# Kernel tuning notes

Measured on AMD Instinct MI355X. Metric: run time of the kernel, lower is better.

Reference implementation:

```python
import jax, jax.numpy as jnp
import numpy as np

B, D, NH, HD = 32, 384, 8, 48
HP = WP = 14
N = HP * WP
L = 24
EPS_LN = 1e-5


def _ln(x, w, b):
    m = jnp.mean(x, -1, keepdims=True)
    v = jnp.mean((x - m) ** 2, -1, keepdims=True)
    return (x - m) * jax.lax.rsqrt(v + EPS_LN) * w + b


def _gelu(x):
    return jax.nn.gelu(x, approximate=False)


def _conv(x, w, s, p, groups=1):
    return jax.lax.conv_general_dilated(x, w, (s, s), [(p, p), (p, p)],
        dimension_numbers=('NCHW', 'OIHW', 'NCHW'), feature_group_count=groups)


def _bn(x, g, b):
    # eval-mode BatchNorm2d with running_mean=0, running_var=1
    scale = g * jax.lax.rsqrt(jnp.asarray(1.0 + 1e-5, x.dtype))
    return x * scale[None, :, None, None] + b[None, :, None, None]


def _pos_embed(pos_w, pos_b):
    two_pi = 2.0 * np.pi
    y = (jnp.arange(HP, dtype=jnp.float32) + 1.0) / ((HP + 1e-6) * two_pi)
    xg = (jnp.arange(WP, dtype=jnp.float32) + 1.0) / ((WP + 1e-6) * two_pi)
    y_embed = jnp.broadcast_to(y[:, None], (HP, WP))
    x_embed = jnp.broadcast_to(xg[None, :], (HP, WP))
    dim_t = 10000.0 ** (2.0 * (jnp.arange(32) // 2).astype(jnp.float32) / 32.0)
    px = x_embed[..., None] / dim_t  # [H,W,32]
    py = y_embed[..., None] / dim_t
    px = jnp.stack([jnp.sin(px[..., 0::2]), jnp.cos(px[..., 1::2])], -1).reshape(HP, WP, 32)
    py = jnp.stack([jnp.sin(py[..., 0::2]), jnp.cos(py[..., 1::2])], -1).reshape(HP, WP, 32)
    pos = jnp.concatenate([py, px], -1)  # [H,W,64]
    pos = jnp.einsum('hwc,dc->hwd', pos, pos_w[:, :, 0, 0]) + pos_b
    return pos.reshape(1, N, D)


def _xca_block(t, p):
    Bc = t.shape[0]
    h = _ln(t, p['n1_w'], p['n1_b'])
    qkv = (h @ p['qkv_w'].T + p['qkv_b']).reshape(Bc, N, 3, NH, HD)
    q = qkv[:, :, 0].transpose(0, 2, 3, 1)  # [B,H,d,N]
    k = qkv[:, :, 1].transpose(0, 2, 3, 1)
    v = qkv[:, :, 2].transpose(0, 2, 3, 1)
    q = q / jnp.maximum(jnp.linalg.norm(q, axis=-1, keepdims=True), 1e-12)
    k = k / jnp.maximum(jnp.linalg.norm(k, axis=-1, keepdims=True), 1e-12)
    attn = jnp.einsum('bhdn,bhen->bhde', q, k) * p['temp'][None, :, None, None]
    a = jax.nn.softmax(attn, -1)  # channel-wise softmax over d_h
    o = jnp.einsum('bhde,bhen->bnhd', a, v).reshape(Bc, N, D)
    o = o @ p['proj_w'].T + p['proj_b']
    t = t + p['g1'] * o
    h = _ln(t, p['n3_w'], p['n3_b']).transpose(0, 2, 1).reshape(Bc, D, HP, WP)
    h = _conv(h, p['lpi1_w'], 1, 1, groups=D) + p['lpi1_b'][None, :, None, None]
    h = _bn(_gelu(h), p['lpi_bn_g'], p['lpi_bn_b'])
    h = _conv(h, p['lpi2_w'], 1, 1, groups=D) + p['lpi2_b'][None, :, None, None]
    t = t + p['g3'] * h.reshape(Bc, D, N).transpose(0, 2, 1)
    h = _ln(t, p['n2_w'], p['n2_b'])
    h = _gelu(h @ p['fc1_w'].T + p['fc1_b']) @ p['fc2_w'].T + p['fc2_b']
    return t + p['g2'] * h


def _ca_block(t, p):
    Bc, Nc, _ = t.shape
    h = _ln(t, p['n1_w'], p['n1_b'])
    qkv = (h @ p['qkv_w'].T + p['qkv_b']).reshape(Bc, Nc, 3, NH, HD)
    q = qkv[:, :, 0].transpose(0, 2, 1, 3)  # [B,H,N,d]
    k = qkv[:, :, 1].transpose(0, 2, 1, 3)
    v = qkv[:, :, 2].transpose(0, 2, 1, 3)
    attn = jnp.sum(q[:, :, :1] * k, -1) * (HD ** -0.5)  # [B,H,N]
    a = jax.nn.softmax(attn, -1)
    cls = jnp.einsum('bhn,bhnd->bhd', a, v).reshape(Bc, 1, D)
    cls = cls @ p['proj_w'].T + p['proj_b']
    attn_out = jnp.concatenate([cls, h[:, 1:]], 1)
    t = t + p['g1'] * attn_out
    t = _ln(t, p['n2_w'], p['n2_b'])
    res = t
    cls2 = _gelu(t[:, :1] @ p['fc1_w'].T + p['fc1_b']) @ p['fc2_w'].T + p['fc2_b']
    return jnp.concatenate([p['g2'] * cls2, t[:, 1:]], 1) + res


def setup_inputs() -> dict:
    key = jax.random.key(0)
    k = iter(jax.random.split(key, 64))
    def rn(shape, std=0.02):
        return jax.random.normal(next(k), shape, jnp.float32) * std
    inp = {}
    inp['x'] = jax.random.normal(next(k), (B, 3, 224, 224), jnp.float32)
    inp['cls_token'] = rn((1, 1, D))
    inp['pos_w'] = rn((D, 64, 1, 1))
    inp['pos_b'] = jnp.zeros((D,))
    for i, (co, ci) in enumerate([(48, 3), (96, 48), (192, 96), (384, 192)], 1):
        inp['pe_w%d' % i] = rn((co, ci, 3, 3))
        inp['pe_g%d' % i] = jnp.ones((co,))
        inp['pe_b%d' % i] = jnp.zeros((co,))
    inp['xqkv_w'] = rn((L, 3 * D, D)); inp['xqkv_b'] = jnp.zeros((L, 3 * D))
    inp['xproj_w'] = rn((L, D, D)); inp['xproj_b'] = jnp.zeros((L, D))
    inp['xtemp'] = jnp.ones((L, NH))
    for n in ('n1', 'n2', 'n3'):
        inp['x%s_w' % n] = jnp.ones((L, D)); inp['x%s_b' % n] = jnp.zeros((L, D))
    inp['xfc1_w'] = rn((L, 4 * D, D)); inp['xfc1_b'] = jnp.zeros((L, 4 * D))
    inp['xfc2_w'] = rn((L, D, 4 * D)); inp['xfc2_b'] = jnp.zeros((L, D))
    inp['xlpi1_w'] = rn((L, D, 1, 3, 3), 0.1); inp['xlpi1_b'] = jnp.zeros((L, D))
    inp['xlpi2_w'] = rn((L, D, 1, 3, 3), 0.1); inp['xlpi2_b'] = jnp.zeros((L, D))
    inp['xbn_g'] = jnp.ones((L, D)); inp['xbn_b'] = jnp.zeros((L, D))
    for g in ('g1', 'g2', 'g3'):
        inp['x%s' % g] = jnp.full((L, D), 1e-5)
    L2 = 2
    inp['cqkv_w'] = rn((L2, 3 * D, D)); inp['cqkv_b'] = jnp.zeros((L2, 3 * D))
    inp['cproj_w'] = rn((L2, D, D)); inp['cproj_b'] = jnp.zeros((L2, D))
    for n in ('n1', 'n2'):
        inp['c%s_w' % n] = jnp.ones((L2, D)); inp['c%s_b' % n] = jnp.zeros((L2, D))
    inp['cfc1_w'] = rn((L2, 4 * D, D)); inp['cfc1_b'] = jnp.zeros((L2, 4 * D))
    inp['cfc2_w'] = rn((L2, D, 4 * D)); inp['cfc2_b'] = jnp.zeros((L2, D))
    inp['cg1'] = jnp.full((L2, D), 1e-5); inp['cg2'] = jnp.full((L2, D), 1e-5)
    inp['norm_w'] = jnp.ones((D,)); inp['norm_b'] = jnp.zeros((D,))
    inp['head_w'] = rn((1000, D)); inp['head_b'] = jnp.zeros((1000,))
    return inp


def reference(x, cls_token, pos_w, pos_b, pe_w1, pe_g1, pe_b1, pe_w2, pe_g2, pe_b2, pe_w3, pe_g3, pe_b3, pe_w4, pe_g4, pe_b4, xqkv_w, xqkv_b, xproj_w, xproj_b, xtemp, xn1_w, xn1_b, xn2_w, xn2_b, xn3_w, xn3_b, xfc1_w, xfc1_b, xfc2_w, xfc2_b, xlpi1_w, xlpi1_b, xlpi2_w, xlpi2_b, xbn_g, xbn_b, xg1, xg2, xg3, cqkv_w, cqkv_b, cproj_w, cproj_b, cn1_w, cn1_b, cn2_w, cn2_b, cfc1_w, cfc1_b, cfc2_w, cfc2_b, cg1, cg2, norm_w, norm_b, head_w, head_b):
    h = _gelu(_bn(_conv(x, pe_w1, 2, 1), pe_g1, pe_b1))
    h = _gelu(_bn(_conv(h, pe_w2, 2, 1), pe_g2, pe_b2))
    h = _gelu(_bn(_conv(h, pe_w3, 2, 1), pe_g3, pe_b3))
    h = _bn(_conv(h, pe_w4, 2, 1), pe_g4, pe_b4)  # [B,D,14,14]
    t = h.reshape(h.shape[0], D, N).transpose(0, 2, 1)  # [B,N,D]
    t = t + _pos_embed(pos_w, pos_b)
    xca = {'qkv_w': xqkv_w, 'qkv_b': xqkv_b, 'proj_w': xproj_w, 'proj_b': xproj_b,
           'temp': xtemp, 'n1_w': xn1_w, 'n1_b': xn1_b, 'n2_w': xn2_w, 'n2_b': xn2_b,
           'n3_w': xn3_w, 'n3_b': xn3_b, 'fc1_w': xfc1_w, 'fc1_b': xfc1_b,
           'fc2_w': xfc2_w, 'fc2_b': xfc2_b, 'lpi1_w': xlpi1_w, 'lpi1_b': xlpi1_b,
           'lpi2_w': xlpi2_w, 'lpi2_b': xlpi2_b, 'lpi_bn_g': xbn_g, 'lpi_bn_b': xbn_b,
           'g1': xg1, 'g2': xg2, 'g3': xg3}
    t, _ = jax.lax.scan(lambda c, p: (_xca_block(c, p), None), t, xca)
    t = jnp.concatenate([jnp.broadcast_to(cls_token, (t.shape[0], 1, D)), t], 1)
    for i in range(2):
        p = {'qkv_w': cqkv_w[i], 'qkv_b': cqkv_b[i], 'proj_w': cproj_w[i],
             'proj_b': cproj_b[i], 'n1_w': cn1_w[i], 'n1_b': cn1_b[i],
             'n2_w': cn2_w[i], 'n2_b': cn2_b[i], 'fc1_w': cfc1_w[i],
             'fc1_b': cfc1_b[i], 'fc2_w': cfc2_w[i], 'fc2_b': cfc2_b[i],
             'g1': cg1[i], 'g2': cg2[i]}
        t = _ca_block(t, p)
    t = _ln(t, norm_w, norm_b)[:, 0]
    return t @ head_w.T + head_b
```

## Files before the change

### kernel.cpp

```cpp
#include <hip/hip_runtime.h>
#include <hip/hip_bf16.h>

#define B_ 32
#define D_ 384
#define N_ 196
#define NH_ 8
#define HD_ 48
#define L_ 24

typedef __bf16 bf16x8 __attribute__((ext_vector_type(8)));
typedef __bf16 bf16x4 __attribute__((ext_vector_type(4)));
typedef float f32x4 __attribute__((ext_vector_type(4)));

__device__ __forceinline__ float gelu_f(float v){
    return 0.5f * v * (1.0f + erff(v * 0.70710678118654752f));
}

__global__ __launch_bounds__(256) void cvt_bf(const float* __restrict__ s, __bf16* __restrict__ d, long n){
    long i = ((long)blockIdx.x * 256 + threadIdx.x) * 8;
    if (i >= n) return;
    float4 a = *reinterpret_cast<const float4*>(s + i);
    float4 b = *reinterpret_cast<const float4*>(s + i + 4);
    bf16x8 r;
    r[0] = (__bf16)a.x; r[1] = (__bf16)a.y; r[2] = (__bf16)a.z; r[3] = (__bf16)a.w;
// ... 84 lines not shown
            int p = i * 256 + tid;
            int r = p >> 2, cq = p & 3;
            *reinterpret_cast<bf16x8*>(Ab + r * 80 + cq * 16) = i ? vaC1 : vaC0;
            *reinterpret_cast<bf16x8*>(Bb + r * 80 + cq * 16) = i ? vwC1 : vwC0;
        }
        __syncthreads();
        int kn = (k0 + 32 < Kpad) ? k0 + 32 : k0;
        bf16x8 vaN0 = loadA(kn, 0), vaN1 = loadA(kn, 1);
        bf16x8 vwN0 = loadB(kn, 0), vwN1 = loadB(kn, 1);
        bf16x8 af[4], bfr[4];
        #pragma unroll
        for (int m = 0; m < 4; m++)
            af[m] = *reinterpret_cast<const bf16x8*>(Ab + (wm * 64 + m * 16 + lo) * 80 + hi * 16);
        #pragma unroll
        for (int n = 0; n < 4; n++)
            bfr[n] = *reinterpret_cast<const bf16x8*>(Bb + (wn * 64 + n * 16 + lo) * 80 + hi * 16);
        #pragma unroll
        for (int m = 0; m < 4; m++)
            #pragma unroll
            for (int n = 0; n < 4; n++)
                acc[m][n] = __builtin_amdgcn_mfma_f32_16x16x32_bf16(af[m], bfr[n], acc[m][n], 0, 0, 0);
        __syncthreads();
        vaC0 = vaN0; vaC1 = vaN1; vwC0 = vwN0; vwC1 = vwN1;
    }
    float* Cf = (float*)Cv;
    __bf16* Cb = (__bf16*)Cv;
    #pragma unroll
    for (int m = 0; m < 4; m++){
        #pragma unroll
        for (int n = 0; n < 4; n++){
            int row = row0 + wm * 64 + m * 16 + hi * 4;
            int col = col0 + wn * 64 + n * 16 + lo;
            if (col >= N) continue;
            float scale = g[col] * rsqrtf(1.0f + 1e-5f);
            float bv = bb[col];
            #pragma unroll
            for (int j = 0; j < 4; j++){
                float v = acc[m][n][j] * scale + bv;
                if (GELU) v = gelu_f(v);
                if (POSOUT)
                    Cf[(long)(row + j) * 384 + col] = v + pos[((row + j) % 196) * 384 + col];
                else
                    Cb[(long)(row + j) * N + col] = (__bf16)v;
            }
        }
    }
}

template<int GELU, int POSOUT, int C, int Hi, int Wi, int Ho, int Wo>
__global__ __launch_bounds__(256) void gemm_cig(const __bf16* __restrict__ in, int Kpad,
                                                const __bf16* __restrict__ W,
                                                const float* __restrict__ g, const float* __restrict__ bb,
                                                void* __restrict__ Cv, int N,
                                                const float* __restrict__ pos){
    __shared__ __align__(16) char smem[36864];
    char* Ab = smem;
    char* Bb = smem + 18432;
    const int tid  = threadIdx.x;
    const int lane = tid & 63;
    const int wn   = (tid >> 6) & 1;
    const int wm   = tid >> 7;
    const int row0 = blockIdx.x * 128;
    const int col0 = blockIdx.y * 128;
    const int hi = lane >> 4, lo = lane & 15;
    f32x4 acc[4][4] = {};
    auto loadA = [&](int kk, int i)->bf16x8 {
        int p = i * 256 + tid;
        int r = p >> 3, cq = p & 7;
        int koff = kk + cq * 8;
        int tap = koff / C;
        int ci = koff - tap * C;
        bf16x8 va{};
        if (tap < 9){
            int pix = row0 + r;
            int b = pix / (Ho * Wo);
            int rem = pix - b * (Ho * Wo);
            int oy = rem / Wo, ox = rem - oy * Wo;
            int iy = oy * 2 - 1 + tap / 3, ix = ox * 2 - 1 + tap % 3;
            if ((unsigned)iy < (unsigned)Hi && (unsigned)ix < (unsigned)Wi)
                va = *reinterpret_cast<const bf16x8*>(in + (((long)b * Hi + iy) * Wi + ix) * C + ci);
        }
        return va;
    };
    auto loadB = [&](int kk, int i)->bf16x8 {
        int p = i * 256 + tid;
        int r = p >> 3, cq = p & 7;
        int gc = col0 + r;
        bf16x8 vw{};
        if (gc < N) vw = *reinterpret_cast<const bf16x8*>(W + (long)gc * Kpad + kk + cq * 8);
        return vw;
    };
    bf16x8 vaC[4], vwC[4];
    #pragma unroll
    for (int i = 0; i < 4; i++){ vaC[i] = loadA(0, i); vwC[i] = loadB(0, i); }
    for (int k0 = 0; k0 < Kpad; k0 += 64){
        #pragma unroll
        for (int i = 0; i < 4; i++){
            int p = i * 256 + tid;
            int r = p >> 3, cq = p & 7;
            *reinterpret_cast<bf16x8*>(Ab + r * 144 + cq * 16) = vaC[i];
            *reinterpret_cast<bf16x8*>(Bb + r * 144 + cq * 16) = vwC[i];
        }
        __syncthreads();
        int kn = (k0 + 64 < Kpad) ? k0 + 64 : k0;
        bf16x8 vaN[4], vwN[4];
        #pragma unroll
        for (int i = 0; i < 4; i++){ vaN[i] = loadA(kn, i); vwN[i] = loadB(kn, i); }
        bf16x8 af[2][4], bfr[2][4];
        #pragma unroll
        for (int m = 0; m < 4; m++){
            af[0][m] = *reinterpret_cast<const bf16x8*>(Ab + (wm * 64 + m * 16 + lo) * 144 + hi * 16);
            af[1][m] = *reinterpret_cast<const bf16x8*>(Ab + (wm * 64 + m * 16 + lo) * 144 + 64 + hi * 16);
        }
        #pragma unroll
        for (int n = 0; n < 4; n++){
            bfr[0][n] = *reinterpret_cast<const bf16x8*>(Bb + (wn * 64 + n * 16 + lo) * 144 + hi * 16);
            bfr[1][n] = *reinterpret_cast<const bf16x8*>(Bb + (wn * 64 + n * 16 + lo) * 144 + 64 + hi * 16);
        }
        #pragma unroll
        for (int kc = 0; kc < 2; kc++)
            #pragma unroll
            for (int m = 0; m < 4; m++)
                #pragma unroll
                for (int n = 0; n < 4; n++)
                    acc[m][n] = __builtin_amdgcn_mfma_f32_16x16x32_bf16(af[kc][m], bfr[kc][n], acc[m][n], 0, 0, 0);
        __syncthreads();
        #pragma unroll
        for (int i = 0; i < 4; i++){ vaC[i] = vaN[i]; vwC[i] = vwN[i]; }
    }
    float* Cf = (float*)Cv;
    __bf16* Cb = (__bf16*)Cv;
    #pragma unroll
    for (int m = 0; m < 4; m++){
        #pragma unroll
        for (int n = 0; n < 4; n++){
            int row = row0 + wm * 64 + m * 16 + hi * 4;
            int col = col0 + wn * 64 + n * 16 + lo;
            if (col >= N) continue;
            float scale = g[col] * rsqrtf(1.0f + 1e-5f);
            float bv = bb[col];
            #pragma unroll
            for (int j = 0; j < 4; j++){
                float v = acc[m][n][j] * scale + bv;
                if (GELU) v = gelu_f(v);
                if (POSOUT)
                    Cf[(long)(row + j) * 384 + col] = v + pos[((row + j) % 196) * 384 + col];
                else
                    Cb[(long)(row + j) * N + col] = (__bf16)v;
            }
        }
    }
}

__global__ __launch_bounds__(128) void ln384(const float* __restrict__ x, long xstride,
                                             const float* __restrict__ w, const float* __restrict__ b,
                                             float* __restrict__ y, long ystride){
    long row = blockIdx.x;
    int tid = threadIdx.x;
    const float* xr = x + row * xstride;
    float v0 = xr[tid], v1 = xr[tid + 128], v2 = xr[tid + 256];
    float s = v0 + v1 + v2;
    float ss = v0 * v0 + v1 * v1 + v2 * v2;
    for (int off = 32; off; off >>= 1){ s += __shfl_down(s, off); ss += __shfl_down(ss, off); }
    __shared__ float rs[2], rss[2];
    if ((tid & 63) == 0){ rs[tid >> 6] = s; rss[tid >> 6] = ss; }
    __syncthreads();
    float S = rs[0] + rs[1], SS = rss[0] + rss[1];
    float m = S * (1.0f / 384.0f);
    float var = SS * (1.0f / 384.0f) - m * m;
    float r = rsqrtf(var + 1e-5f);
    float* yr = y + row * ystride;
    yr[tid]       = (v0 - m) * r * w[tid]       + b[tid];
    yr[tid + 128] = (v1 - m) * r * w[tid + 128] + b[tid + 128];
    yr[tid + 256] = (v2 - m) * r * w[tid + 256] + b[tid + 256];
}

__global__ __launch_bounds__(128) void ln384_bf(const float* __restrict__ x,
                                                const float* __restrict__ w, const float* __restrict__ b,
                                                __bf16* __restrict__ y){
    long row = blockIdx.x;
    int tid = threadIdx.x;
    const float* xr = x + row * 384;
    float v0 = xr[tid], v1 = xr[tid + 128], v2 = xr[tid + 256];
    float s = v0 + v1 + v2;
    float ss = v0 * v0 + v1 * v1 + v2 * v2;
    for (int off = 32; off; off >>= 1){ s += __shfl_down(s, off); ss += __shfl_down(ss, off); }
    __shared__ float rs[2], rss[2];
    if ((tid & 63) == 0){ rs[tid >> 6] = s; rss[tid >> 6] = ss; }
    __syncthreads();
    float S = rs[0] + rs[1], SS = rss[0] + rss[1];
    float m = S * (1.0f / 384.0f);
    float var = SS * (1.0f / 384.0f) - m * m;
    float r = rsqrtf(var + 1e-5f);
    __bf16* yr = y + row * 384;
    yr[tid]       = (__bf16)((v0 - m) * r * w[tid]       + b[tid]);
    yr[tid + 128] = (__bf16)((v1 - m) * r * w[tid + 128] + b[tid + 128]);
    yr[tid + 256] = (__bf16)((v2 - m) * r * w[tid + 256] + b[tid + 256]);
}

__global__ __launch_bounds__(128) void proj_res_lnt(const __bf16* __restrict__ o2,
                                                    const float* __restrict__ g1,
                                                    float* __restrict__ t,
                                                    const float* __restrict__ n3w, const float* __restrict__ n3b,
                                                    __bf16* __restrict__ ht){
    long row = blockIdx.x;
    int tid = threadIdx.x;
    int c0 = tid * 4;
    float v[4] = {0.f, 0.f, 0.f, 0.f};
    if (tid < 96){
        float4 tv = *reinterpret_cast<const float4*>(t + row * 384 + c0);
        bf16x4 ov = *reinterpret_cast<const bf16x4*>(o2 + row * 384 + c0);
        v[0] = tv.x + g1[c0 + 0] * (float)ov[0];
        v[1] = tv.y + g1[c0 + 1] * (float)ov[1];
        v[2] = tv.z + g1[c0 + 2] * (float)ov[2];
        v[3] = tv.w + g1[c0 + 3] * (float)ov[3];
        *reinterpret_cast<float4*>(t + row * 384 + c0) = make_float4(v[0], v[1], v[2], v[3]);
    }
    float s = v[0] + v[1] + v[2] + v[3];
    float ss = v[0] * v[0] + v[1] * v[1] + v[2] * v[2] + v[3] * v[3];
    for (int off = 32; off; off >>= 1){ s += __shfl_down(s, off); ss += __shfl_down(ss, off); }
    __shared__ float rs[2], rss[2];
    if ((tid & 63) == 0){ rs[tid >> 6] = s; rss[tid >> 6] = ss; }
    __syncthreads();
    float S = rs[0] + rs[1], SS = rss[0] + rss[1];
    float m = S * (1.0f / 384.0f);
    float var = SS * (1.0f / 384.0f) - m * m;
    float r = rsqrtf(var + 1e-5f);
    if (tid < 96){
        int b = (int)(row / 196), n = (int)(row % 196);
        __bf16* yb = ht + ((long)b * 384) * 196 + n;
        #pragma unroll
        for (int j = 0; j < 4; j++){
            int c = c0 + j;
            yb[(long)c * 196] = (__bf16)((v[j] - m) * r * n3w[c] + n3b[c]);
        }
    }
}

__global__ __launch_bounds__(128) void ln2res(float* __restrict__ t,
                                              const __bf16* __restrict__ hadd,
                                              const float* __restrict__ n2w, const float* __restrict__ n2b,
                                              __bf16* __restrict__ h){
    long row = blockIdx.x;
    int tid = threadIdx.x;
    int c0 = tid * 4;
    float v[4] = {0.f, 0.f, 0.f, 0.f};
    if (tid < 96){
        float4 tv = *reinterpret_cast<const float4*>(t + row * 384 + c0);
        bf16x4 hv = *reinterpret_cast<const bf16x4*>(hadd + row * 384 + c0);
        v[0] = tv.x + (float)hv[0];
        v[1] = tv.y + (float)hv[1];
        v[2] = tv.z + (float)hv[2];
        v[3] = tv.w + (float)hv[3];
        *reinterpret_cast<float4*>(t + row * 384 + c0) = make_float4(v[0], v[1], v[2], v[3]);
    }
    float s = v[0] + v[1] + v[2] + v[3];
    float ss = v[0] * v[0] + v[1] * v[1] + v[2] * v[2] + v[3] * v[3];
    for (int off = 32; off; off >>= 1){ s += __shfl_down(s, off); ss += __shfl_down(ss, off); }
    __shared__ float rs[2], rss[2];
    if ((tid & 63) == 0){ rs[tid >> 6] = s; rss[tid >> 6] = ss; }
    __syncthreads();
    float S = rs[0] + rs[1], SS = rss[0] + rss[1];
    float m = S * (1.0f / 384.0f);
    float var = SS * (1.0f / 384.0f) - m * m;
    float r = rsqrtf(var + 1e-5f);
    if (tid < 96){
        bf16x4 o;
        #pragma unroll
        for (int j = 0; j < 4; j++){
            int c = c0 + j;
            o[j] = (__bf16)((v[j] - m) * r * n2w[c] + n2b[c]);
        }
        *reinterpret_cast<bf16x4*>(h + row * 384 + c0) = o;
    }
}

__global__ __launch_bounds__(128) void fc2_res_ln(const __bf16* __restrict__ f2,
                                                  const float* __restrict__ g2,
                                                  float* __restrict__ t,
                                                  const float* __restrict__ n1w, const float* __restrict__ n1b,
                                                  __bf16* __restrict__ h){
    long row = blockIdx.x;
    int tid = threadIdx.x;
    int c0 = tid * 4;
    float v[4] = {0.f, 0.f, 0.f, 0.f};
    if (tid < 96){
        float4 tv = *reinterpret_cast<const float4*>(t + row * 384 + c0);
        bf16x4 fv = *reinterpret_cast<const bf16x4*>(f2 + row * 384 + c0);
        v[0] = tv.x + g2[c0 + 0] * (float)fv[0];
        v[1] = tv.y + g2[c0 + 1] * (float)fv[1];
        v[2] = tv.z + g2[c0 + 2] * (float)fv[2];
        v[3] = tv.w + g2[c0 + 3] * (float)fv[3];
        *reinterpret_cast<float4*>(t + row * 384 + c0) = make_float4(v[0], v[1], v[2], v[3]);
    }
    float s = v[0] + v[1] + v[2] + v[3];
    float ss = v[0] * v[0] + v[1] * v[1] + v[2] * v[2] + v[3] * v[3];
    for (int off = 32; off; off >>= 1){ s += __shfl_down(s, off); ss += __shfl_down(ss, off); }
    __shared__ float rs[2], rss[2];
    if ((tid & 63) == 0){ rs[tid >> 6] = s; rss[tid >> 6] = ss; }
    __syncthreads();
    float S = rs[0] + rs[1], SS = rss[0] + rss[1];
    float m = S * (1.0f / 384.0f);
    float var = SS * (1.0f / 384.0f) - m * m;
    float r = rsqrtf(var + 1e-5f);
    if (tid < 96){
        bf16x4 o;
// ... 101 lines not shown
        for (int n = 0; n < 2; n++){
            int row = row0 + m * 16 + hi * 4;
            int col = col0 + wn * 32 + n * 16 + lo;
            if (NGUARD && col >= Ncols) continue;
            float bv = bias[col];
            #pragma unroll
            for (int j = 0; j < 4; j++){
                if (GUARD && (row + j) >= M) continue;
                float v = acc[m][n][j] + bv;
                if (MODE == 1) v = gelu_f(v);
                long ci = (long)(row + j) * ldc + col;
                if (OUTBF) Cb[ci] = (__bf16)v;
                else Cf[ci] = v;
            }
        }
    }
}

__global__ __launch_bounds__(256) void gemm_bb3(const __bf16* __restrict__ A, long lda,
                                                const __bf16* __restrict__ W, int Kw,
                                                const float* __restrict__ bias,
                                                __bf16* __restrict__ C, long ldc,
                                                int K){
    __shared__ __align__(16) char smem[18432];
    char* Ab = smem;
    char* Bb = smem + 9216;
    const int tid = threadIdx.x;
    const int lane = tid & 63;
    const int wid = tid >> 6;
    const int wm = wid >> 1, wnn = wid & 1;
    const int row0 = blockIdx.x * 64;
    const int col0 = blockIdx.y * 64;
    const int hi = lane >> 4, lo = lane & 15;
    f32x4 acc[2][2] = {};
    auto loadA = [&](int kk, int i)->bf16x8 {
        int p = i * 256 + tid;
        int r = p >> 3, cq = p & 7;
        return *reinterpret_cast<const bf16x8*>(A + (long)(row0 + r) * lda + kk + cq * 8);
    };
    auto loadB = [&](int kk, int i)->bf16x8 {
        int p = i * 256 + tid;
        int r = p >> 3, cq = p & 7;
        return *reinterpret_cast<const bf16x8*>(W + (long)(col0 + r) * Kw + kk + cq * 8);
    };
    bf16x8 vaC[2], vwC[2];
    vaC[0] = loadA(0, 0); vaC[1] = loadA(0, 1);
    vwC[0] = loadB(0, 0); vwC[1] = loadB(0, 1);
    for (int k0 = 0; k0 < K; k0 += 64){
        #pragma unroll
        for (int i = 0; i < 2; i++){
            int p = i * 256 + tid;
            int r = p >> 3, cq = p & 7;
            *reinterpret_cast<bf16x8*>(Ab + r * 144 + cq * 16) = vaC[i];
            *reinterpret_cast<bf16x8*>(Bb + r * 144 + cq * 16) = vwC[i];
        }
        __syncthreads();
        int kn = (k0 + 64 < K) ? k0 + 64 : k0;
        bf16x8 vaN[2], vwN[2];
        vaN[0] = loadA(kn, 0); vaN[1] = loadA(kn, 1);
        vwN[0] = loadB(kn, 0); vwN[1] = loadB(kn, 1);
        bf16x8 af[2][2], bfr[2][2];
        #pragma unroll
        for (int m = 0; m < 2; m++){
            af[0][m] = *reinterpret_cast<const bf16x8*>(Ab + (wm * 32 + m * 16 + lo) * 144 + hi * 16);
            af[1][m] = *reinterpret_cast<const bf16x8*>(Ab + (wm * 32 + m * 16 + lo) * 144 + 64 + hi * 16);
        }
        #pragma unroll
        for (int n = 0; n < 2; n++){
            bfr[0][n] = *reinterpret_cast<const bf16x8*>(Bb + (wnn * 32 + n * 16 + lo) * 144 + hi * 16);
            bfr[1][n] = *reinterpret_cast<const bf16x8*>(Bb + (wnn * 32 + n * 16 + lo) * 144 + 64 + hi * 16);
        }
        #pragma unroll
        for (int kc = 0; kc < 2; kc++)
            #pragma unroll
            for (int m = 0; m < 2; m++)
                #pragma unroll
                for (int n = 0; n < 2; n++)
                    acc[m][n] = __builtin_amdgcn_mfma_f32_16x16x32_bf16(af[kc][m], bfr[kc][n], acc[m][n], 0, 0, 0);
        __syncthreads();
        vaC[0] = vaN[0]; vaC[1] = vaN[1]; vwC[0] = vwN[0]; vwC[1] = vwN[1];
    }
    #pragma unroll
    for (int m = 0; m < 2; m++){
        #pragma unroll
        for (int n = 0; n < 2; n++){
            int row = row0 + wm * 32 + m * 16 + hi * 4;
            int col = col0 + wnn * 32 + n * 16 + lo;
            float bv = bias[col];
            #pragma unroll
            for (int j = 0; j < 4; j++)
                C[(long)(row + j) * ldc + col] = (__bf16)(acc[m][n][j] + bv);
        }
    }
}

__global__ __launch_bounds__(384) void pos_embed(const float* __restrict__ pw, const float* __restrict__ pb,
                                                 float* __restrict__ pos){
    __shared__ float p64[64];
    int n = blockIdx.x;
    int iy = n / 14, ix = n % 14;
    int t = threadIdx.x;
    if (t < 64){
        int axis = t >> 5;
        int c = t & 31;
        int u = c >> 1;
        float coord = (axis == 0) ? (float)(iy + 1) : (float)(ix + 1);
        float val = coord / ((14.0f + 1e-6f) * 6.283185307179586f);
        float T = powf(10000.0f, (float)u / 16.0f);
        float a = val / T;
        p64[t] = (c & 1) ? cosf(a) : sinf(a);
    }
    __syncthreads();
    float acc = 0.f;
    const float* wr = pw + (long)t * 64;
    #pragma unroll 8
    for (int c = 0; c < 64; c++) acc += p64[c] * wr[c];
    pos[n * 384 + t] = acc + pb[t];
}

__global__ __launch_bounds__(256) void xca2(const __bf16* __restrict__ qkv, const float* __restrict__ temp,
                                            __bf16* __restrict__ o){
    __shared__ __align__(16) char smem[45056];
    __bf16* qs = (__bf16*)smem;
    __bf16* ks = (__bf16*)(smem + 22272);
    float* inq = (float*)(smem + 44544);
    float* ink = (float*)(smem + 44736);
    float* att = (float*)smem;
    __bf16* abf = (__bf16*)(smem + 22272);
    int bh = blockIdx.x;
    int b = bh >> 3, h = bh & 7;
    const int tid = threadIdx.x;
    const int wid = tid >> 6, lane = tid & 63;
    const int hi = lane >> 4, lo = lane & 15;
    const __bf16* base = qkv + ((long)b * 196) * 1152 + h * 48;
    bf16x8 z8 = {};
    for (int idx = tid; idx < 48 * 28; idx += 256){
        int d = idx / 28, n = 196 + idx % 28;
        qs[d * 232 + n] = (__bf16)0.f;
        ks[d * 232 + n] = (__bf16)0.f;
    }
    for (int ch = tid; ch < 196 * 6; ch += 256){
        int n = ch / 6, c = ch % 6, d0 = c * 8;
        bf16x8 q8 = *reinterpret_cast<const bf16x8*>(base + (long)n * 1152 + d0);
        bf16x8 k8 = *reinterpret_cast<const bf16x8*>(base + (long)n * 1152 + 384 + d0);
        #pragma unroll
        for (int j = 0; j < 8; j++){
            qs[(d0 + j) * 232 + n] = q8[j];
            ks[(d0 + j) * 232 + n] = k8[j];
        }
    }
    __syncthreads();
    for (int r = wid; r < 48; r += 4){
        float sq = 0.f, sk = 0.f;
        for (int n = lane; n < 196; n += 64){
            float qv = (float)qs[r * 232 + n];
            float kv = (float)ks[r * 232 + n];
            sq += qv * qv; sk += kv * kv;
        }
        for (int off = 32; off; off >>= 1){ sq += __shfl_down(sq, off); sk += __shfl_down(sk, off); }
        if (lane == 0){
            inq[r] = 1.0f / fmaxf(sqrtf(sq), 1e-12f);
            ink[r] = 1.0f / fmaxf(sqrtf(sk), 1e-12f);
        }
    }
    __syncthreads();
    float tempv = temp[h];
    f32x4 qk0 = {}, qk1 = {}, qk2 = {};
    __builtin_amdgcn_s_setprio(1);
    {
        int mi = wid / 3, ni = wid % 3;
        #pragma unroll
        for (int k0 = 0; k0 < 224; k0 += 32){
            bf16x8 af = *reinterpret_cast<const bf16x8*>(qs + (mi * 16 + lo) * 232 + k0 + hi * 8);
            bf16x8 bf = *reinterpret_cast<const bf16x8*>(ks + (ni * 16 + lo) * 232 + k0 + hi * 8);
            qk0 = __builtin_amdgcn_mfma_f32_16x16x32_bf16(af, bf, qk0, 0, 0, 0);
        }
    }
    {
        int tt = wid + 4;
        int mi = tt / 3, ni = tt % 3;
        #pragma unroll
        for (int k0 = 0; k0 < 224; k0 += 32){
            bf16x8 af = *reinterpret_cast<const bf16x8*>(qs + (mi * 16 + lo) * 232 + k0 + hi * 8);
            bf16x8 bf = *reinterpret_cast<const bf16x8*>(ks + (ni * 16 + lo) * 232 + k0 + hi * 8);
            qk1 = __builtin_amdgcn_mfma_f32_16x16x32_bf16(af, bf, qk1, 0, 0, 0);
        }
    }
    if (wid == 0){
        #pragma unroll
        for (int k0 = 0; k0 < 224; k0 += 32){
            bf16x8 af = *reinterpret_cast<const bf16x8*>(qs + (2 * 16 + lo) * 232 + k0 + hi * 8);
            bf16x8 bf = *reinterpret_cast<const bf16x8*>(ks + (2 * 16 + lo) * 232 + k0 + hi * 8);
            qk2 = __builtin_amdgcn_mfma_f32_16x16x32_bf16(af, bf, qk2, 0, 0, 0);
        }
    }
    __builtin_amdgcn_s_setprio(0);
    __syncthreads();
    {
        int mi = wid / 3, ni = wid % 3;
        int e = ni * 16 + lo;
        float se = ink[e] * tempv;
        #pragma unroll
        for (int j = 0; j < 4; j++){
            int d = mi * 16 + hi * 4 + j;
            att[d * 68 + e] = qk0[j] * inq[d] * se;
        }
    }
    {
        int tt = wid + 4;
        int mi = tt / 3, ni = tt % 3;
        int e = ni * 16 + lo;
        float se = ink[e] * tempv;
        #pragma unroll
        for (int j = 0; j < 4; j++){
            int d = mi * 16 + hi * 4 + j;
            att[d * 68 + e] = qk1[j] * inq[d] * se;
        }
    }
    if (wid == 0){
        int e = 2 * 16 + lo;
        float se = ink[e] * tempv;
        #pragma unroll
        for (int j = 0; j < 4; j++){
            int d = 2 * 16 + hi * 4 + j;
            att[d * 68 + e] = qk2[j] * inq[d] * se;
        }
    }
    __syncthreads();
    if (tid < 192){
        int r = tid >> 2, q4 = tid & 3;
        const float* row = att + r * 68 + q4 * 12;
        float mx = -1e30f;
        #pragma unroll
        for (int i = 0; i < 12; i++) mx = fmaxf(mx, row[i]);
        mx = fmaxf(mx, __shfl_xor(mx, 1));
        mx = fmaxf(mx, __shfl_xor(mx, 2));
        float pv[12]; float sm = 0.f;
        #pragma unroll
        for (int i = 0; i < 12; i++){ pv[i] = expf(row[i] - mx); sm += pv[i]; }
        sm += __shfl_xor(sm, 1);
        sm += __shfl_xor(sm, 2);
        float inv = 1.0f / sm;
        #pragma unroll
        for (int i = 0; i < 12; i++) abf[r * 72 + q4 * 12 + i] = (__bf16)(pv[i] * inv);
    }
    for (int idx = tid; idx < 48 * 3; idx += 256){
        int r = idx / 3, c = 48 + (idx % 3) * 8;
        *reinterpret_cast<bf16x8*>(abf + r * 72 + c) = z8;
    }
    __syncthreads();
    __bf16* ob = o + ((long)b * 196) * 384 + h * 48;
    __builtin_amdgcn_s_setprio(1);
    for (int tt = wid; tt < 39; tt += 4){
        int mi = tt / 13, ni = tt % 13;
        int nB = ni * 16 + lo;
        const __bf16* vrow = base + (long)nB * 1152 + 768;
        f32x4 acc = {};
        #pragma unroll
        for (int e0 = 0; e0 < 64; e0 += 32){
            bf16x8 af = *reinterpret_cast<const bf16x8*>(abf + (mi * 16 + lo) * 72 + e0 + hi * 8);
            bf16x8 bf = *reinterpret_cast<const bf16x8*>(vrow + e0 + hi * 8);
            acc = __builtin_amdgcn_mfma_f32_16x16x32_bf16(af, bf, acc, 0, 0, 0);
        }
        int n = nB;
        if (n < 196){
            #pragma unroll
            for (int j = 0; j < 4; j++){
                int d = mi * 16 + hi * 4 + j;
                ob[(long)n * 384 + d] = (__bf16)acc[j];
            }
        }
    }
    __builtin_amdgcn_s_setprio(0);
}

__global__ __launch_bounds__(256) void lpi_g(const __bf16* __restrict__ ht,
                                             const float* __restrict__ w1, const float* __restrict__ b1,
                                             const float* __restrict__ bng, const float* __restrict__ bnb,
                                             const float* __restrict__ w2, const float* __restrict__ b2,
                                             const float* __restrict__ g3, __bf16* __restrict__ hadd){
    int bd = blockIdx.x;
    int d = bd % 384, b = bd / 384;
    __shared__ float p[16][16];
    __shared__ float p2[16][16];
    __shared__ float wA[9], wB[9];
    int tt = threadIdx.x;
    int yy = tt / 16, xx = tt % 16;
    p[yy][xx] = 0.f; p2[yy][xx] = 0.f;
    if (tt < 9){ wA[tt] = w1[d * 9 + tt]; wB[tt] = w2[d * 9 + tt]; }
    __syncthreads();
    if (tt < 196){
        int y = tt / 14, x = tt % 14;
        p[y + 1][x + 1] = (float)ht[((long)b * 384 + d) * 196 + tt];
    }
    __syncthreads();
    if (tt < 196){
        int y = tt / 14, x = tt % 14;
        float a = 0.f;
        #pragma unroll
        for (int ky = 0; ky < 3; ky++)
            #pragma unroll
            for (int kx = 0; kx < 3; kx++)
                a += wA[ky * 3 + kx] * p[y + ky][x + kx];
        a += b1[d];
        a = gelu_f(a);
        a = a * (bng[d] * rsqrtf(1.0f + 1e-5f)) + bnb[d];
        p2[y + 1][x + 1] = a;
    }
    __syncthreads();
    if (tt < 196){
        int y = tt / 14, x = tt % 14;
        float a = 0.f;
        #pragma unroll
        for (int ky = 0; ky < 3; ky++)
            #pragma unroll
            for (int kx = 0; kx < 3; kx++)
                a += wB[ky * 3 + kx] * p2[y + ky][x + kx];
        a += b2[d];
        hadd[((long)b * 196 + tt) * 384 + d] = (__bf16)(g3[d] * a);
    }
}

__global__ __launch_bounds__(256) void concat_cls(const float* __restrict__ t, const float* __restrict__ clstok,
                                                  float* __restrict__ tc){
    long i = (long)blockIdx.x * 256 + threadIdx.x;
    if (i >= (long)B_ * 197 * 384) return;
    int d = (int)(i % 384);
    long bn = i / 384;
    int n = (int)(bn % 197);
    int b = (int)(bn / 197);
    tc[i] = (n == 0) ? clstok[d] : t[((long)b * 196 + (n - 1)) * 384 + d];
}

__global__ __launch_bounds__(256) void ca_attn(const __bf16* __restrict__ qkv, float* __restrict__ clsp){
    int bh = blockIdx.x;
    int b = bh >> 3, h = bh & 7;
    const __bf16* base = qkv + (long)b * 197 * 1152 + h * 48;
    __shared__ float q0[48];
    __shared__ float at2[197];
    __shared__ float smax, ssum;
    int tid = threadIdx.x;
    if (tid < 48) q0[tid] = (float)base[tid];
    __syncthreads();
    if (tid < 197){
        const __bf16* kr = base + (long)tid * 1152 + 384;
        float s = 0.f;
        for (int d = 0; d < 48; d++) s += q0[d] * (float)kr[d];
        at2[tid] = s * rsqrtf(48.0f);
    }
    __syncthreads();
    if (tid == 0){
        float m = -1e30f;
        for (int n = 0; n < 197; n++) m = fmaxf(m, at2[n]);
        smax = m;
    }
    __syncthreads();
    if (tid < 197) at2[tid] = expf(at2[tid] - smax);
    __syncthreads();
    if (tid == 0){
        float s = 0.f;
        for (int n = 0; n < 197; n++) s += at2[n];
        ssum = s;
    }
    __syncthreads();
    if (tid < 48){
        const __bf16* vb = base + 768 + tid;
        float s = 0.f;
        for (int n = 0; n < 197; n++) s += at2[n] * (float)vb[(long)n * 1152];
        clsp[b * 384 + h * 48 + tid] = s / ssum;
    }
}

__global__ __launch_bounds__(256) void ca_update1(const float* __restrict__ clso, const float* __restrict__ hc,
                                                  const float* __restrict__ g1, float* __restrict__ tc){
    long i = (long)blockIdx.x * 256 + threadIdx.x;
    if (i >= (long)B_ * 197 * 384) return;
    int d = (int)(i % 384);
    long bn = i / 384;
    int n = (int)(bn % 197);
    int b = (int)(bn / 197);
    float add = (n == 0) ? clso[b * 384 + d] : hc[i];
    tc[i] += g1[d] * add;
}

__global__ __launch_bounds__(256) void ca_update2(const float* __restrict__ cls2, const float* __restrict__ hc,
                                                  const float* __restrict__ g2, float* __restrict__ tc){
    long i = (long)blockIdx.x * 256 + threadIdx.x;
    if (i >= (long)B_ * 197 * 384) return;
    int d = (int)(i % 384);
    long bn = i / 384;
    int n = (int)(bn % 197);
    int b = (int)(bn / 197);
    float hv = hc[i];
    tc[i] = (n == 0) ? (g2[d] * cls2[b * 384 + d] + hv) : (hv + hv);
}

extern "C" void kernel_launch(void* const* d_in, const int* in_sizes, int n_in,
                              void* d_out, int out_size, void* d_ws, size_t ws_size,
                              hipStream_t stream){
    (void)in_sizes; (void)n_in; (void)out_size; (void)ws_size;
    const float* x      = (const float*)d_in[0];
    const float* clstok = (const float*)d_in[1];
    const float* pos_w  = (const float*)d_in[2];
    const float* pos_b  = (const float*)d_in[3];
    const float* pe_w[4] = {(const float*)d_in[4], (const float*)d_in[7], (const float*)d_in[10], (const float*)d_in[13]};
    const float* pe_g[4] = {(const float*)d_in[5], (const float*)d_in[8], (const float*)d_in[11], (const float*)d_in[14]};
    const float* pe_b[4] = {(const float*)d_in[6], (const float*)d_in[9], (const float*)d_in[12], (const float*)d_in[15]};
    const float* xqkv_w = (const float*)d_in[16];
    const float* xqkv_b = (const float*)d_in[17];
    const float* xproj_w = (const float*)d_in[18];
    const float* xproj_b = (const float*)d_in[19];
    const float* xtemp  = (const float*)d_in[20];
    const float* xn1_w = (const float*)d_in[21];
    const float* xn1_b = (const float*)d_in[22];
    const float* xn2_w = (const float*)d_in[23];
    const float* xn2_b = (const float*)d_in[24];
    const float* xn3_w = (const float*)d_in[25];
    const float* xn3_b = (const float*)d_in[26];
    const float* xfc1_w = (const float*)d_in[27];
    const float* xfc1_b = (const float*)d_in[28];
    const float* xfc2_w = (const float*)d_in[29];
    const float* xfc2_b = (const float*)d_in[30];
    const float* xlpi1_w = (const float*)d_in[31];
    const float* xlpi1_b = (const float*)d_in[32];
    const float* xlpi2_w = (const float*)d_in[33];
    const float* xlpi2_b = (const float*)d_in[34];
    const float* xbn_g = (const float*)d_in[35];
    const float* xbn_b = (const float*)d_in[36];
    const float* xg1 = (const float*)d_in[37];
    const float* xg2 = (const float*)d_in[38];
    const float* xg3 = (const float*)d_in[39];
    const float* cqkv_w = (const float*)d_in[40];
    const float* cqkv_b = (const float*)d_in[41];
    const float* cproj_w = (const float*)d_in[42];
    const float* cproj_b = (const float*)d_in[43];
    const float* cn1_w = (const float*)d_in[44];
    const float* cn1_b = (const float*)d_in[45];
    const float* cn2_w = (const float*)d_in[46];
    const float* cn2_b = (const float*)d_in[47];
    const float* cfc1_w = (const float*)d_in[48];
    const float* cfc1_b = (const float*)d_in[49];
    const float* cfc2_w = (const float*)d_in[50];
    const float* cfc2_b = (const float*)d_in[51];
    const float* cg1 = (const float*)d_in[52];
    const float* cg2 = (const float*)d_in[53];
    const float* norm_w = (const float*)d_in[54];
    const float* norm_b = (const float*)d_in[55];
    const float* head_w = (const float*)d_in[56];
    const float* head_b = (const float*)d_in[57];
    float* outp = (float*)d_out;

    float* ws = (float*)d_ws;
    __bf16* A1   = (__bf16*)(ws);
    __bf16* out1 = (__bf16*)(ws + 7000000L);
    __bf16* out2 = (__bf16*)(ws + 17000000L);
    __bf16* out3 = (__bf16*)(ws + 25000000L);
    __bf16* wcv  = (__bf16*)(ws + 36000000L);
    __bf16* W1c = wcv;
    __bf16* W2c = wcv + 1536;
    __bf16* W3c = wcv + 44544;
    __bf16* W4c = wcv + 216576;
    __bf16* wqkv_bf = (__bf16*)(ws);
    __bf16* wproj_bf = (__bf16*)(ws + 5308416L);
    __bf16* wfc1_bf = (__bf16*)(ws + 7077888L);
    __bf16* wfc2_bf = (__bf16*)(ws + 14155776L);
    float*  t       = ws + 21233664L;
    float*  pos     = ws + 23642112L;
    __bf16* h_bf    = (__bf16*)(ws + 23717376L);
    __bf16* qkv_bf  = (__bf16*)(ws + 24921600L);
    __bf16* o_bf    = (__bf16*)(ws + 28534272L);
    __bf16* ht_bf   = (__bf16*)(ws + 29738496L);
    __bf16* f1_bf   = (__bf16*)(ws + 32146944L);
    __bf16* o2_bf   = (__bf16*)(ws + 34555392L);
    __bf16* f2_bf   = (__bf16*)(ws + 24921600L);
    __bf16* hadd_bf = (__bf16*)(ws + 28534272L);
    float* tc   = ws;
    float* hc   = ws + 2420736L;
    __bf16* qkvc_bf = (__bf16*)(ws + 4841472L);
    float* clsp = ws + 8472576L;
    float* clso = clsp + 12288;
    float* f1c  = clso + 12288;
    float* cls2 = f1c + 49152;
    float* clsf = cls2 + 12288;
    __bf16* cqkv_bf  = (__bf16*)(ws + 9000000L);
    __bf16* cproj_bf = (__bf16*)(ws + 9500000L);
    __bf16* cfc1_bf  = (__bf16*)(ws + 9800000L);
    __bf16* cfc2_bf  = (__bf16*)(ws + 10400000L);
    __bf16* headw_bf = (__bf16*)(ws + 11000000L);

    wprep<<<(48 * 32 + 255) / 256, 256, 0, stream>>>(pe_w[0], W1c, 48, 3, 32);
    wprep<<<(96 * 448 + 255) / 256, 256, 0, stream>>>(pe_w[1], W2c, 96, 48, 448);
    wprep<<<(192 * 896 + 255) / 256, 256, 0, stream>>>(pe_w[2], W3c, 192, 96, 896);
    wprep<<<(384 * 1728 + 255) / 256, 256, 0, stream>>>(pe_w[3], W4c, 384, 192, 1728);

    im2col_x<<<1568, 256, 0, stream>>>(x, A1);
    { dim3 g(3136, 1); gemm_conv<1, 0><<<g, 256, 0, stream>>>(A1, 32, W1c, pe_g[0], pe_b[0], out1, 48, nullptr); }
    pos_embed<<<196, 384, 0, stream>>>(pos_w, pos_b, pos);
    { dim3 g(784, 1);
      gemm_cig<1, 0, 48, 112, 112, 56, 56><<<g, 256, 0, stream>>>(out1, 448, W2c, pe_g[1], pe_b[1], out2, 96, nullptr); }
    { dim3 g(196, 2);
      gemm_cig<1, 0, 96, 56, 56, 28, 28><<<g, 256, 0, stream>>>(out2, 896, W3c, pe_g[2], pe_b[2], out3, 192, nullptr); }
    { dim3 g(49, 3);
      gemm_cig<0, 1, 192, 28, 28, 14, 14><<<g, 256, 0, stream>>>(out3, 1728, W4c, pe_g[3], pe_b[3], t, 384, pos); }

    {
        long n1 = (long)L_ * 1152 * 384;
        long n2 = (long)L_ * 384 * 384;
        long n3 = (long)L_ * 1536 * 384;
        cvt_bf<<<(int)((n1 + 2047) / 2048), 256, 0, stream>>>(xqkv_w, wqkv_bf, n1);
        cvt_bf<<<(int)((n2 + 2047) / 2048), 256, 0, stream>>>(xproj_w, wproj_bf, n2);
        cvt_bf<<<(int)((n3 + 2047) / 2048), 256, 0, stream>>>(xfc1_w, wfc1_bf, n3);
        cvt_bf<<<(int)((n3 + 2047) / 2048), 256, 0, stream>>>(xfc2_w, wfc2_bf, n3);
    }

    const int M = B_ * N_;
    ln384_bf<<<M, 128, 0, stream>>>(t, xn1_w, xn1_b, h_bf);
    for (int l = 0; l < L_; l++){
        {
            dim3 g(98, 9);
            gemm_bb2<0, 1, 0, 0, 0><<<g, 256, 0, stream>>>(h_bf, 384, wqkv_bf + (long)l * 1152 * 384, 384,
                                                           xqkv_b + l * 1152, qkv_bf, 1152, 384, M, 0);
        }
        xca2<<<B_ * NH_, 256, 0, stream>>>(qkv_bf, xtemp + l * 8, o_bf);
        {
            dim3 g(98, 6);
            gemm_bb3<<<g, 256, 0, stream>>>(o_bf, 384, wproj_bf + (long)l * 384 * 384, 384,
                                            xproj_b + l * 384, o2_bf, 384, 384);
        }
        proj_res_lnt<<<M, 128, 0, stream>>>(o2_bf, xg1 + l * 384, t,
                                            xn3_w + l * 384, xn3_b + l * 384, ht_bf);
        lpi_g<<<B_ * D_, 256, 0, stream>>>(ht_bf, xlpi1_w + (long)l * 384 * 9, xlpi1_b + l * 384,
                                           xbn_g + l * 384, xbn_b + l * 384,
                                           xlpi2_w + (long)l * 384 * 9, xlpi2_b + l * 384,
                                           xg3 + l * 384, hadd_bf);
        ln2res<<<M, 128, 0, stream>>>(t, hadd_bf, xn2_w + l * 384, xn2_b + l * 384, h_bf);
        {
            dim3 g(98, 12);
            gemm_bb2<1, 1, 0, 0, 0><<<g, 256, 0, stream>>>(h_bf, 384, wfc1_bf + (long)l * 1536 * 384, 384,
                                                           xfc1_b + l * 1536, f1_bf, 1536, 384, M, 0);
        }
        {
            dim3 g(98, 6);
            gemm_bb3<<<g, 256, 0, stream>>>(f1_bf, 1536, wfc2_bf + (long)l * 1536 * 384, 1536,
                                            xfc2_b + l * 384, f2_bf, 384, 1536);
        }
        int ln = (l + 1) % L_;
        fc2_res_ln<<<M, 128, 0, stream>>>(f2_bf, xg2 + l * 384, t,
                                          xn1_w + ln * 384, xn1_b + ln * 384, h_bf);
    }

    const long NC = (long)B_ * 197 * 384;
    concat_cls<<<(int)(NC / 256), 256, 0, stream>>>(t, clstok, tc);
    {
        long nc = (long)2 * 1152 * 384;
        cvt_bf<<<(int)((nc + 2047) / 2048), 256, 0, stream>>>(cqkv_w, cqkv_bf, nc);
        long np = (long)2 * 384 * 384;
        cvt_bf<<<(int)((np + 2047) / 2048), 256, 0, stream>>>(cproj_w, cproj_bf, np);
        long nf = (long)2 * 1536 * 384;
        cvt_bf<<<(int)((nf + 2047) / 2048), 256, 0, stream>>>(cfc1_w, cfc1_bf, nf);
        cvt_bf<<<(int)((nf + 2047) / 2048), 256, 0, stream>>>(cfc2_w, cfc2_bf, nf);
        cvt_pad<<<(1024 * 384 + 255) / 256, 256, 0, stream>>>(head_w, headw_bf, 1000, 384, 1024);
    }
    const int MC = B_ * 197;
    for (int i = 0; i < 2; i++){
        ln384<<<MC, 128, 0, stream>>>(tc, 384, cn1_w + i * 384, cn1_b + i * 384, hc, 384);
        {
            dim3 g(99, 9);
            gemm_bb2<0, 1, 1, 1, 0><<<g, 256, 0, stream>>>(hc, 384, cqkv_bf + (long)i * 1152 * 384, 384,
                                                           cqkv_b + i * 1152, qkvc_bf, 1152, 384, MC, 0);
        }
        ca_attn<<<B_ * NH_, 256, 0, stream>>>(qkvc_bf, clsp);
        {
            dim3 g(1, 3);
            gemm_bb2<0, 0, 1, 1, 0><<<g, 256, 0, stream>>>(clsp, 384, cproj_bf + (long)i * 384 * 384, 384,
                                                           cproj_b + i * 384, clso, 384, 384, 32, 0);
        }
        ca_update1<<<(int)(NC / 256), 256, 0, stream>>>(clso, hc, cg1 + i * 384, tc);
        ln384<<<MC, 128, 0, stream>>>(tc, 384, cn2_w + i * 384, cn2_b + i * 384, hc, 384);
        {
            dim3 g(1, 12);
            gemm_bb2<1, 0, 1, 1, 0><<<g, 256, 0, stream>>>(hc, (long)197 * 384, cfc1_bf + (long)i * 1536 * 384, 384,
                                                           cfc1_b + i * 1536, f1c, 1536, 384, 32, 0);
        }
        {
            dim3 g(1, 3);
            gemm_bb2<0, 0, 1, 1, 0><<<g, 256, 0, stream>>>(f1c, 1536, cfc2_bf + (long)i * 1536 * 384, 1536,
                                                           cfc2_b + i * 384, cls2, 384, 1536, 32, 0);
        }
        ca_update2<<<(int)(NC / 256), 256, 0, stream>>>(cls2, hc, cg2 + i * 384, tc);
    }

    ln384<<<32, 128, 0, stream>>>(tc, (long)197 * 384, norm_w, norm_b, clsf, 384);
    {
        dim3 g(1, 8);
        gemm_bb2<0, 0, 1, 1, 1><<<g, 256, 0, stream>>>(clsf, 384, headw_bf, 384,
                                                       head_b, outp, 1000, 384, 32, 1000);
    }
}
```

Before: 3.778 ms.

## Use 128x128 register-prefetched GEMM for QKV/FC1 and bf16 class-attention activations

Adds a new 128x128-tile bf16 GEMM kernel that prefetches the next K-slice into registers while computing from LDS, and uses it for the per-layer QKV and FC1 projections in place of the smaller-tile kernel. The q/k norm reduction in XCA now uses vectorized 4-wide LDS reads. The class-attention stage stores its LayerNorm output as bf16 instead of fp32, which halves that traffic and feeds the GEMMs directly. The larger tiles halve the grid and use more registers, and the bf16 residual path in ca_update changes numerics slightly.

```diff
diff --git a/kernel.cpp b/kernel.cpp
--- a/kernel.cpp
+++ b/kernel.cpp
@@ -260,6 +260,88 @@
     }
 }
 
+template<int MODE>
+__global__ __launch_bounds__(256) void gemm_bb4(const __bf16* __restrict__ A, long lda,
+                                                const __bf16* __restrict__ W, int Kw,
+                                                const float* __restrict__ bias,
+                                                __bf16* __restrict__ C, long ldc,
+                                                int K){
+    __shared__ __align__(16) char smem[36864];
+    char* Ab = smem;
+    char* Bb = smem + 18432;
+    const int tid  = threadIdx.x;
+    const int lane = tid & 63;
+    const int wn   = (tid >> 6) & 1;
+    const int wm   = tid >> 7;
+    const int row0 = blockIdx.x * 128;
+    const int col0 = blockIdx.y * 128;
+    const int hi = lane >> 4, lo = lane & 15;
+    f32x4 acc[4][4] = {};
+    auto loadA = [&](int kk, int i)->bf16x8 {
+        int p = i * 256 + tid;
+        int r = p >> 3, cq = p & 7;
+        return *reinterpret_cast<const bf16x8*>(A + (long)(row0 + r) * lda + kk + cq * 8);
+    };
+    auto loadB = [&](int kk, int i)->bf16x8 {
+        int p = i * 256 + tid;
+        int r = p >> 3, cq = p & 7;
+        return *reinterpret_cast<const bf16x8*>(W + (long)(col0 + r) * Kw + kk + cq * 8);
+    };
+    bf16x8 vaC[4], vwC[4];
+    #pragma unroll
+    for (int i = 0; i < 4; i++){ vaC[i] = loadA(0, i); vwC[i] = loadB(0, i); }
+    for (int k0 = 0; k0 < K; k0 += 64){
+        #pragma unroll
+        for (int i = 0; i < 4; i++){
+            int p = i * 256 + tid;
+            int r = p >> 3, cq = p & 7;
+            *reinterpret_cast<bf16x8*>(Ab + r * 144 + cq * 16) = vaC[i];
+            *reinterpret_cast<bf16x8*>(Bb + r * 144 + cq * 16) = vwC[i];
+        }
+        __syncthreads();
+        int kn = (k0 + 64 < K) ? k0 + 64 : k0;
+        bf16x8 vaN[4], vwN[4];
+        #pragma unroll
+        for (int i = 0; i < 4; i++){ vaN[i] = loadA(kn, i); vwN[i] = loadB(kn, i); }
+        bf16x8 af[2][4], bfr[2][4];
+        #pragma unroll
+        for (int m = 0; m < 4; m++){
+            af[0][m] = *reinterpret_cast<const bf16x8*>(Ab + (wm * 64 + m * 16 + lo) * 144 + hi * 16);
+            af[1][m] = *reinterpret_cast<const bf16x8*>(Ab + (wm * 64 + m * 16 + lo) * 144 + 64 + hi * 16);
+        }
+        #pragma unroll
+        for (int n = 0; n < 4; n++){
+            bfr[0][n] = *reinterpret_cast<const bf16x8*>(Bb + (wn * 64 + n * 16 + lo) * 144 + hi * 16);
+            bfr[1][n] = *reinterpret_cast<const bf16x8*>(Bb + (wn * 64 + n * 16 + lo) * 144 + 64 + hi * 16);
+        }
+        #pragma unroll
+        for (int kc = 0; kc < 2; kc++)
+            #pragma unroll
+            for (int m = 0; m < 4; m++)
+                #pragma unroll
+                for (int n = 0; n < 4; n++)
+                    acc[m][n] = __builtin_amdgcn_mfma_f32_16x16x32_bf16(af[kc][m], bfr[kc][n], acc[m][n], 0, 0, 0);
+        __syncthreads();
+        #pragma unroll
+        for (int i = 0; i < 4; i++){ vaC[i] = vaN[i]; vwC[i] = vwN[i]; }
+    }
+    #pragma unroll
+    for (int m = 0; m < 4; m++){
+        #pragma unroll
+        for (int n = 0; n < 4; n++){
+            int row = row0 + wm * 64 + m * 16 + hi * 4;
+            int col = col0 + wn * 64 + n * 16 + lo;
+            float bv = bias[col];
+            #pragma unroll
+            for (int j = 0; j < 4; j++){
+                float v = acc[m][n][j] + bv;
+                if (MODE == 1) v = gelu_f(v);
+                C[(long)(row + j) * ldc + col] = (__bf16)v;
+            }
+        }
+    }
+}
+
 __global__ __launch_bounds__(128) void ln384(const float* __restrict__ x, long xstride,
                                              const float* __restrict__ w, const float* __restrict__ b,
                                              float* __restrict__ y, long ystride){
@@ -667,10 +749,14 @@
     __syncthreads();
     for (int r = wid; r < 48; r += 4){
         float sq = 0.f, sk = 0.f;
-        for (int n = lane; n < 196; n += 64){
-            float qv = (float)qs[r * 232 + n];
-            float kv = (float)ks[r * 232 + n];
-            sq += qv * qv; sk += kv * kv;
+        if (lane < 56){
+            bf16x4 q4 = *reinterpret_cast<const bf16x4*>(qs + r * 232 + lane * 4);
+            bf16x4 k4 = *reinterpret_cast<const bf16x4*>(ks + r * 232 + lane * 4);
+            #pragma unroll
+            for (int j = 0; j < 4; j++){
+                float qv = (float)q4[j], kv = (float)k4[j];
+                sq += qv * qv; sk += kv * kv;
+            }
         }
         for (int off = 32; off; off >>= 1){ sq += __shfl_down(sq, off); sk += __shfl_down(sk, off); }
         if (lane == 0){
@@ -886,7 +972,7 @@
     }
 }
 
-__global__ __launch_bounds__(256) void ca_update1(const float* __restrict__ clso, const float* __restrict__ hc,
+__global__ __launch_bounds__(256) void ca_update1(const float* __restrict__ clso, const __bf16* __restrict__ hc,
                                                   const float* __restrict__ g1, float* __restrict__ tc){
     long i = (long)blockIdx.x * 256 + threadIdx.x;
     if (i >= (long)B_ * 197 * 384) return;
@@ -894,11 +980,11 @@
     long bn = i / 384;
     int n = (int)(bn % 197);
     int b = (int)(bn / 197);
-    float add = (n == 0) ? clso[b * 384 + d] : hc[i];
+    float add = (n == 0) ? clso[b * 384 + d] : (float)hc[i];
     tc[i] += g1[d] * add;
 }
 
-__global__ __launch_bounds__(256) void ca_update2(const float* __restrict__ cls2, const float* __restrict__ hc,
+__global__ __launch_bounds__(256) void ca_update2(const float* __restrict__ cls2, const __bf16* __restrict__ hc,
                                                   const float* __restrict__ g2, float* __restrict__ tc){
     long i = (long)blockIdx.x * 256 + threadIdx.x;
     if (i >= (long)B_ * 197 * 384) return;
@@ -906,7 +992,7 @@
     long bn = i / 384;
     int n = (int)(bn % 197);
     int b = (int)(bn / 197);
-    float hv = hc[i];
+    float hv = (float)hc[i];
     tc[i] = (n == 0) ? (g2[d] * cls2[b * 384 + d] + hv) : (hv + hv);
 }
 
@@ -990,7 +1076,7 @@
     __bf16* f2_bf   = (__bf16*)(ws + 24921600L);
     __bf16* hadd_bf = (__bf16*)(ws + 28534272L);
     float* tc   = ws;
-    float* hc   = ws + 2420736L;
+    __bf16* hc_bf = (__bf16*)(ws + 2420736L);
     __bf16* qkvc_bf = (__bf16*)(ws + 4841472L);
     float* clsp = ws + 8472576L;
     float* clso = clsp + 12288;
@@ -1032,9 +1118,9 @@
     ln384_bf<<<M, 128, 0, stream>>>(t, xn1_w, xn1_b, h_bf);
     for (int l = 0; l < L_; l++){
         {
-            dim3 g(98, 9);
-            gemm_bb2<0, 1, 0, 0, 0><<<g, 256, 0, stream>>>(h_bf, 384, wqkv_bf + (long)l * 1152 * 384, 384,
-                                                           xqkv_b + l * 1152, qkv_bf, 1152, 384, M, 0);
+            dim3 g(49, 9);
+            gemm_bb4<0><<<g, 256, 0, stream>>>(h_bf, 384, wqkv_bf + (long)l * 1152 * 384, 384,
+                                               xqkv_b + l * 1152, qkv_bf, 1152, 384);
         }
         xca2<<<B_ * NH_, 256, 0, stream>>>(qkv_bf, xtemp + l * 8, o_bf);
         {
@@ -1050,9 +1136,9 @@
                                            xg3 + l * 384, hadd_bf);
         ln2res<<<M, 128, 0, stream>>>(t, hadd_bf, xn2_w + l * 384, xn2_b + l * 384, h_bf);
         {
-            dim3 g(98, 12);
-            gemm_bb2<1, 1, 0, 0, 0><<<g, 256, 0, stream>>>(h_bf, 384, wfc1_bf + (long)l * 1536 * 384, 384,
-                                                           xfc1_b + l * 1536, f1_bf, 1536, 384, M, 0);
+            dim3 g(49, 12);
+            gemm_bb4<1><<<g, 256, 0, stream>>>(h_bf, 384, wfc1_bf + (long)l * 1536 * 384, 384,
+                                               xfc1_b + l * 1536, f1_bf, 1536, 384);
         }
         {
             dim3 g(98, 6);
@@ -1078,10 +1164,10 @@
     }
     const int MC = B_ * 197;
     for (int i = 0; i < 2; i++){
-        ln384<<<MC, 128, 0, stream>>>(tc, 384, cn1_w + i * 384, cn1_b + i * 384, hc, 384);
+        ln384_bf<<<MC, 128, 0, stream>>>(tc, cn1_w + i * 384, cn1_b + i * 384, hc_bf);
         {
             dim3 g(99, 9);
-            gemm_bb2<0, 1, 1, 1, 0><<<g, 256, 0, stream>>>(hc, 384, cqkv_bf + (long)i * 1152 * 384, 384,
+            gemm_bb2<0, 1, 0, 1, 0><<<g, 256, 0, stream>>>(hc_bf, 384, cqkv_bf + (long)i * 1152 * 384, 384,
                                                            cqkv_b + i * 1152, qkvc_bf, 1152, 384, MC, 0);
         }
         ca_attn<<<B_ * NH_, 256, 0, stream>>>(qkvc_bf, clsp);
@@ -1090,11 +1176,11 @@
             gemm_bb2<0, 0, 1, 1, 0><<<g, 256, 0, stream>>>(clsp, 384, cproj_bf + (long)i * 384 * 384, 384,
                                                            cproj_b + i * 384, clso, 384, 384, 32, 0);
         }
-        ca_update1<<<(int)(NC / 256), 256, 0, stream>>>(clso, hc, cg1 + i * 384, tc);
-        ln384<<<MC, 128, 0, stream>>>(tc, 384, cn2_w + i * 384, cn2_b + i * 384, hc, 384);
+        ca_update1<<<(int)(NC / 256), 256, 0, stream>>>(clso, hc_bf, cg1 + i * 384, tc);
+        ln384_bf<<<MC, 128, 0, stream>>>(tc, cn2_w + i * 384, cn2_b + i * 384, hc_bf);
         {
             dim3 g(1, 12);
-            gemm_bb2<1, 0, 1, 1, 0><<<g, 256, 0, stream>>>(hc, (long)197 * 384, cfc1_bf + (long)i * 1536 * 384, 384,
+            gemm_bb2<1, 0, 0, 1, 0><<<g, 256, 0, stream>>>(hc_bf, (long)197 * 384, cfc1_bf + (long)i * 1536 * 384, 384,
                                                            cfc1_b + i * 1536, f1c, 1536, 384, 32, 0);
         }
         {
@@ -1102,7 +1188,7 @@
             gemm_bb2<0, 0, 1, 1, 0><<<g, 256, 0, stream>>>(f1c, 1536, cfc2_bf + (long)i * 1536 * 384, 1536,
                                                            cfc2_b + i * 384, cls2, 384, 1536, 32, 0);
         }
-        ca_update2<<<(int)(NC / 256), 256, 0, stream>>>(cls2, hc, cg2 + i * 384, tc);
+        ca_update2<<<(int)(NC / 256), 256, 0, stream>>>(cls2, hc_bf, cg2 + i * 384, tc);
     }
 
     ln384<<<32, 128, 0, stream>>>(tc, (long)197 * 384, norm_w, norm_b, clsf, 384);
```

Result: slower. 3.942 ms (+4.4%).
